# Optimization experiments

Measured on AMD Instinct MI355X. Metric: run time of the kernel, lower is better.

Reference implementation:

```python
import jax, jax.numpy as jnp
import numpy as np

B = 128      # batch
HW = 224     # image height/width
P = 16       # patch size
D = 512      # token_dim
NH = 8       # n_heads
L = 6        # t_blocks
M = 2048     # mlp_layer_size
NC = 10      # output classes
GP = HW // P            # patches per side
T = GP * GP + 1         # tokens incl. class token (197)
EPS = 1e-5


def _ln(x, g, b):
    m = jnp.mean(x, axis=-1, keepdims=True)
    v = jnp.mean(jnp.square(x - m), axis=-1, keepdims=True)
    return (x - m) / jnp.sqrt(v + EPS) * g + b


def setup_inputs() -> dict:
    key = jax.random.key(0)
    ks = iter(jax.random.split(key, 32))
    s = 0.02
    inp = {
        "images": jax.random.normal(next(ks), (B, 1, HW, HW), dtype=jnp.float32),
        "lin_map_w": jax.random.normal(next(ks), (D, P * P), dtype=jnp.float32) * s,
        "lin_map_b": jnp.zeros((D,), jnp.float32),
        "class_token": jax.random.uniform(next(ks), (1, D), dtype=jnp.float32),
        "ln1_g": jnp.ones((L, D), jnp.float32),
        "ln1_b": jnp.zeros((L, D), jnp.float32),
        "ln2_g": jnp.ones((L, D), jnp.float32),
        "ln2_b": jnp.zeros((L, D), jnp.float32),
        "qw": jax.random.normal(next(ks), (L, NH, D, D), dtype=jnp.float32) * s,
        "qb": jnp.zeros((L, NH, D), jnp.float32),
        "kw": jax.random.normal(next(ks), (L, NH, D, D), dtype=jnp.float32) * s,
        "kb": jnp.zeros((L, NH, D), jnp.float32),
        "vw": jax.random.normal(next(ks), (L, NH, D, D), dtype=jnp.float32) * s,
        "vb": jnp.zeros((L, NH, D), jnp.float32),
        "map_w": jax.random.normal(next(ks), (L, T, T * NH), dtype=jnp.float32) * s,
        "map_b": jnp.zeros((L, T), jnp.float32),
        "mlp_w1": jax.random.normal(next(ks), (L, M, D), dtype=jnp.float32) * s,
        "mlp_b1": jnp.zeros((L, M), jnp.float32),
        "mlp_w2": jax.random.normal(next(ks), (L, D, M), dtype=jnp.float32) * s,
        "mlp_b2": jnp.zeros((L, D), jnp.float32),
        "cls_w": jax.random.normal(next(ks), (NC, D), dtype=jnp.float32) * s,
        "cls_b": jnp.zeros((NC,), jnp.float32),
    }
    return inp


def reference(images, lin_map_w, lin_map_b, class_token, ln1_g, ln1_b, ln2_g, ln2_b,
              qw, qb, kw, kb, vw, vb, map_w, map_b,
              mlp_w1, mlp_b1, mlp_w2, mlp_b2, cls_w, cls_b):
    n = images.shape[0]
    img = images[:, 0]  # (B, HW, HW), channel squeezed as in patching_func
    # non-overlapping patch extraction (patchify with step=patch_size)
    patches = img.reshape(n, GP, P, GP, P).transpose(0, 1, 3, 2, 4).reshape(n, GP * GP, P * P)
    emb = patches @ lin_map_w.T + lin_map_b                 # (B, nP, D)
    cls = jnp.broadcast_to(class_token, (n, 1, D))
    x = jnp.concatenate([cls, emb], axis=1)                 # (B, T, D)
    scale = 1.0 / np.sqrt(T - 1)                            # quirky scale from source
    for l in range(L):
        h = _ln(x, ln1_g[l], ln1_b[l])
        q = jnp.einsum('btd,hed->bhte', h, qw[l]) + qb[l][None, :, None, :]
        k = jnp.einsum('btd,hed->bhte', h, kw[l]) + kb[l][None, :, None, :]
        v = jnp.einsum('btd,hed->bhte', h, vw[l]) + vb[l][None, :, None, :]
        attn = jax.nn.softmax(jnp.einsum('bhte,bhse->bhts', q, k) * scale, axis=-1)
        av = jnp.einsum('bhts,bhse->bhte', attn, v)         # (B, NH, T, D)
        res = av.reshape(n, NH * T, D)                      # head-major concat along tokens
        msa = jnp.einsum('bmd,tm->btd', res, map_w[l]) + map_b[l][None, :, None]
        x = x + msa
        y = _ln(x, ln2_g[l], ln2_b[l])
        mlp = jax.nn.gelu(y @ mlp_w1[l].T + mlp_b1[l], approximate=False) @ mlp_w2[l].T + mlp_b2[l]
        x = y + mlp                                         # note: residual uses ln2(x), per source
    logits = x[:, 0] @ cls_w.T + cls_b
    return jax.nn.softmax(logits, axis=-1)
```

## Files before the change

### kernel.cpp

```cpp
#include <hip/hip_runtime.h>
#include <hip/hip_bf16.h>
#include <math.h>

#define B_   128
#define HW_  224
#define P_   16
#define D_   512
#define NH_  8
#define L_   6
#define M_   2048
#define NC_  10
#define GP_  14
#define T_   197
#define TP_  224
#define EPS_ 1e-5f
#define ZVW2_ 2048
#define RCW_ 448

typedef __hip_bfloat16 bf16;
typedef __attribute__((ext_vector_type(8))) __bf16 bf16x8;
typedef __attribute__((ext_vector_type(4))) float  f32x4;

__device__ __forceinline__ void gload16(const void* g, void* l) {
    __builtin_amdgcn_global_load_lds(
        (const __attribute__((address_space(1))) void*)g,
        (__attribute__((address_space(3))) void*)l, 16, 0, 0);
}


__global__ void k_f32_to_bf16v(const float* __restrict__ in, bf16* __restrict__ out, long n8) {
    long stride = (long)gridDim.x * blockDim.x;
    for (long i = (long)blockIdx.x * blockDim.x + threadIdx.x; i < n8; i += stride) {
        float4 a = ((const float4*)in)[i * 2], b = ((const float4*)in)[i * 2 + 1];
        union { uint4 u; bf16 h[8]; } r;
        r.h[0] = __float2bfloat16(a.x); r.h[1] = __float2bfloat16(a.y);
        r.h[2] = __float2bfloat16(a.z); r.h[3] = __float2bfloat16(a.w);
        r.h[4] = __float2bfloat16(b.x); r.h[5] = __float2bfloat16(b.y);
        r.h[6] = __float2bfloat16(b.z); r.h[7] = __float2bfloat16(b.w);
        ((uint4*)out)[i] = r.u;
    }
}

__global__ void k_f32_to_bf16v2(const float* __restrict__ in1, bf16* __restrict__ out1,
                                const float* __restrict__ in2, bf16* __restrict__ out2, long n8) {
    long stride = (long)gridDim.x * blockDim.x;
    for (long i = (long)blockIdx.x * blockDim.x + threadIdx.x; i < n8; i += stride) {
        {
            float4 a = ((const float4*)in1)[i * 2], b = ((const float4*)in1)[i * 2 + 1];
            union { uint4 u; bf16 h[8]; } r;
            r.h[0] = __float2bfloat16(a.x); r.h[1] = __float2bfloat16(a.y);
            r.h[2] = __float2bfloat16(a.z); r.h[3] = __float2bfloat16(a.w);
            r.h[4] = __float2bfloat16(b.x); r.h[5] = __float2bfloat16(b.y);
            r.h[6] = __float2bfloat16(b.z); r.h[7] = __float2bfloat16(b.w);
            ((uint4*)out1)[i] = r.u;
        }
        {
            float4 a = ((const float4*)in2)[i * 2], b = ((const float4*)in2)[i * 2 + 1];
            union { uint4 u; bf16 h[8]; } r;
            r.h[0] = __float2bfloat16(a.x); r.h[1] = __float2bfloat16(a.y);
            r.h[2] = __float2bfloat16(a.z); r.h[3] = __float2bfloat16(a.w);
            r.h[4] = __float2bfloat16(b.x); r.h[5] = __float2bfloat16(b.y);
            r.h[6] = __float2bfloat16(b.z); r.h[7] = __float2bfloat16(b.w);
            ((uint4*)out2)[i] = r.u;
        }
    }
}

__global__ void k_prep_wv(const float* __restrict__ vw, bf16* __restrict__ wzv) {
    int idx = blockIdx.x * blockDim.x + threadIdx.x;
    if (idx >= NH_ * D_ * (D_ / 8)) return;
    int d8 = idx & 63;
    int e  = (idx >> 6) & 511;
    int h  = idx >> 15;
    long so = ((long)(h * D_ + e)) * D_ + d8 * 8;
    float4 a = *(const float4*)(vw + so), b = *(const float4*)(vw + so + 4);
    union { uint4 u; bf16 hh[8]; } rr;
    rr.hh[0] = __float2bfloat16(a.x); rr.hh[1] = __float2bfloat16(a.y);
    rr.hh[2] = __float2bfloat16(a.z); rr.hh[3] = __float2bfloat16(a.w);
    rr.hh[4] = __float2bfloat16(b.x); rr.hh[5] = __float2bfloat16(b.y);
    rr.hh[6] = __float2bfloat16(b.z); rr.hh[7] = __float2bfloat16(b.w);
    ((uint4*)wzv)[((long)(h * 1024 + 512 + e)) * 64 + d8] = rr.u;
}

__global__ __launch_bounds__(256) void k_prep_ub(const float* __restrict__ kw,
        const float* __restrict__ qb, const float* __restrict__ vb, float* __restrict__ out) {
    int gw = blockIdx.x * 4 + (threadIdx.x >> 6);
    int lane = threadIdx.x & 63;
    if (gw < NH_ * 512) {
        int h = gw >> 9, j = gw & 511;
        const float* kwh = kw + (long)h * D_ * D_ + j;
        const float* qbh = qb + h * D_;
        float s = 0.f;
#pragma unroll
        for (int i = 0; i < 8; i++) {
            int e = i * 64 + lane;
            s += kwh[(long)e * D_] * qbh[e];
        }
#pragma unroll
        for (int off = 32; off; off >>= 1) s += __shfl_xor(s, off, 64);
        if (lane == 0) out[h * 1024 + j] = s;
    } else {
        int t = (gw - NH_ * 512) * 64 + lane;
        if (t < NH_ * 512) {
            int h = t >> 9, j = t & 511;
            out[h * 1024 + 512 + j] = vb[h * D_ + j];
        }
    }
}

__global__ void k_patchify(const float* __restrict__ img, bf16* __restrict__ patches) {
    long idx = (long)blockIdx.x * blockDim.x + threadIdx.x;
    long total = (long)B_ * 196 * 256;
    if (idx >= total) return;
    int q = (int)(idx & 255);
    int p = (int)((idx >> 8) % 196);
    int b = (int)(idx / (196 * 256));
    int gy = p / GP_, gx = p % GP_;
    int py = q >> 4,  px = q & 15;
    patches[idx] = __float2bfloat16(img[((long)b * HW_ + gy * P_ + py) * HW_ + gx * P_ + px]);
}

__global__ void k_cls_token(const float* __restrict__ tok, float* __restrict__ x) {
    int i = blockIdx.x * blockDim.x + threadIdx.x;
    if (i < B_ * D_) {
        int b = i >> 9, d = i & 511;
        x[(long)b * T_ * D_ + d] = tok[d];
    }
}

__global__ void k_prep_map(const float* __restrict__ in, bf16* __restrict__ out) {
    int idx = blockIdx.x * blockDim.x + threadIdx.x;
    int total = NH_ * T_ * TP_;
    if (idx >= total) return;
    int s = idx % TP_;
    int t = (idx / TP_) % T_;
    int h = idx / (TP_ * T_);
    float v = (s < T_) ? in[t * (T_ * NH_) + h * T_ + s] : 0.f;
    out[idx] = __float2bfloat16(v);
}


template<int WRITE_Y>
__global__ __launch_bounds__(256) void k_ln(const float* x,
        const float* __restrict__ g, const float* __restrict__ bb,
        bf16* __restrict__ obf, float* of, int rows) {
    int wid = blockIdx.x * 4 + (threadIdx.x >> 6);
    if (wid >= rows) return;
    int lane = threadIdx.x & 63;
    const float* xr = x + (long)wid * D_;
    float v[8];
    float s = 0.f;
#pragma unroll
    for (int i = 0; i < 8; i++) { v[i] = xr[i * 64 + lane]; s += v[i]; }
#pragma unroll
    for (int off = 32; off; off >>= 1) s += __shfl_xor(s, off, 64);
    float mean = s * (1.f / D_);
    float sq = 0.f;
#pragma unroll
    for (int i = 0; i < 8; i++) { float d = v[i] - mean; sq += d * d; }
#pragma unroll
    for (int off = 32; off; off >>= 1) sq += __shfl_xor(sq, off, 64);
    float inv = rsqrtf(sq * (1.f / D_) + EPS_);
#pragma unroll
    for (int i = 0; i < 8; i++) {
        int d = i * 64 + lane;
        float val = (v[i] - mean) * inv * g[d] + bb[d];
        obf[(long)wid * D_ + d] = __float2bfloat16(val);
        if (WRITE_Y) of[(long)wid * D_ + d] = val;
    }
}


__global__ __launch_bounds__(256) void k_attn_ssm2(
        const bf16* __restrict__ Qbase, long ldq, long qImg, long qHead,
        const bf16* __restrict__ Kbase, long ldk, long kImg,
        bf16* __restrict__ Pm, float scale) {
    __shared__ __align__(16) bf16 Qs[128][32];
    __shared__ __align__(16) bf16 Ks[256][32];
    int z = blockIdx.z;
    int img = z & 127, h2 = z >> 7;
    int q0 = blockIdx.y * 128;
    int tid = threadIdx.x;
    int wv = tid >> 6, lane = tid & 63;

    const bf16* Qp = Qbase + (long)img * qImg + (long)h2 * qHead;
    const bf16* Kp = Kbase + (long)img * kImg;

    int sRow = 16 * wv + (lane >> 2);
    int sCol = ((lane & 3) ^ ((lane >> 3) & 3)) * 8;
    const bf16* gQ = Qp + (long)(q0 + sRow) * ldq + sCol;
    const bf16* gK = Kp + (long)sRow * ldk + sCol;
    char* lQ = (char*)Qs + (16 * wv) * 64;
    char* lK = (char*)Ks + (16 * wv) * 64;

    f32x4 acc[2][13];
#pragma unroll
    for (int j = 0; j < 2; j++)
#pragma unroll
        for (int f = 0; f < 13; f++) acc[j][f] = (f32x4){0.f, 0.f, 0.f, 0.f};

    int kgrp = lane >> 4;
#pragma unroll
    for (int kt = 0; kt < 16; kt++) {
        long k0 = (long)kt * 32;
        gload16(gQ + k0, lQ);
        gload16(gQ + 64 * ldq + k0, lQ + 4096);
#pragma unroll
        for (int p = 0; p < 4; p++)
            gload16(gK + (long)(p * 64) * ldk + k0, lK + p * 4096);
        __syncthreads();
        bf16x8 af[2];
#pragma unroll
        for (int j = 0; j < 2; j++) {
            int R = wv * 32 + j * 16 + (lane & 15);
            af[j] = *(const bf16x8*)&Qs[R][(kgrp ^ ((R >> 1) & 3)) * 8];
        }
#pragma unroll
        for (int f = 0; f < 13; f++) {
            int R = f * 16 + (lane & 15);
            bf16x8 bfr = *(const bf16x8*)&Ks[R][(kgrp ^ ((R >> 1) & 3)) * 8];
            acc[0][f] = __builtin_amdgcn_mfma_f32_16x16x32_bf16(af[0], bfr, acc[0][f], 0, 0, 0);
            acc[1][f] = __builtin_amdgcn_mfma_f32_16x16x32_bf16(af[1], bfr, acc[1][f], 0, 0, 0);
        }
        __syncthreads();
    }

    int c1 = lane & 15, grp = lane >> 4;
    const bf16 z0 = __float2bfloat16(0.f);
#pragma unroll
    for (int j = 0; j < 2; j++) {
        float mx[4] = {-1e30f, -1e30f, -1e30f, -1e30f};
        float sm[4] = {0.f, 0.f, 0.f, 0.f};
#pragma unroll
        for (int f = 0; f < 13; f++) {
            bool val = (f * 16 + c1 < T_);
#pragma unroll
            for (int r = 0; r < 4; r++) {
                float v = val ? acc[j][f][r] * scale : -1e30f;
                acc[j][f][r] = v;
                mx[r] = fmaxf(mx[r], v);
            }
        }
#pragma unroll
        for (int r = 0; r < 4; r++)
#pragma unroll
            for (int off = 1; off < 16; off <<= 1) mx[r] = fmaxf(mx[r], __shfl_xor(mx[r], off, 64));
#pragma unroll
        for (int f = 0; f < 13; f++) {
            bool val = (f * 16 + c1 < T_);
#pragma unroll
            for (int r = 0; r < 4; r++) {
                float e = val ? expf(acc[j][f][r] - mx[r]) : 0.f;
                acc[j][f][r] = e;
                sm[r] += e;
            }
        }
#pragma unroll
        for (int r = 0; r < 4; r++) {
#pragma unroll
            for (int off = 1; off < 16; off <<= 1) sm[r] += __shfl_xor(sm[r], off, 64);
            sm[r] = 1.f / sm[r];
        }
#pragma unroll
        for (int r = 0; r < 4; r++) {
            int qi = q0 + wv * 32 + j * 16 + grp * 4 + r;
            if (qi >= T_) continue;
            bf16* prow = Pm + ((long)z * T_ + qi) * TP_;
#pragma unroll
            for (int f = 0; f < 13; f++)
                prow[f * 16 + c1] = __float2bfloat16(acc[j][f][r] * sm[r]);
            prow[208 + c1] = z0;
        }
    }
}


__device__ __forceinline__ float geluf(float v) {
    return 0.5f * v * (1.f + erff(v * 0.70710678118654752f));
}

template<int MODE, bool GUARD, bool SWZ, int KT>
__global__ __launch_bounds__(256) void k_gemm_bt(
        const bf16* __restrict__ A, long lda, long bsA,
        const bf16* __restrict__ Bw, long ldb, long bsB,
        void* __restrict__ Cp, long ldc, long bsC,
        const float* __restrict__ bias,
        const float* res, long ldres,
        int Mt, int Nt) {
    __shared__ __align__(16) bf16 As[128][32];
    __shared__ __align__(16) bf16 Bs[128][32];
    int bz = blockIdx.z;
    A  += (long)bz * bsA;
    Bw += (long)bz * bsB;

    unsigned bx = blockIdx.x, by = blockIdx.y;
    if (SWZ) {
        unsigned nx = gridDim.x;
        unsigned nwg = nx * gridDim.y;
        unsigned f = by * nx + bx;
        unsigned q = nwg >> 3, r = nwg & 7;
        unsigned xcd = f & 7, idx = f >> 3;
        unsigned base = (xcd < r) ? xcd * (q + 1) : r * (q + 1) + (xcd - r) * q;
        unsigned nf = base + idx;
        bx = nf % nx;
        by = nf / nx;
    }
    int m0 = by * 128, n0 = bx * 128;

    int tid = threadIdx.x;
    int wv = tid >> 6, lane = tid & 63;
    int wm = (wv >> 1) * 64, wn = (wv & 1) * 64;
    int lrow = lane & 15, kgrp = lane >> 4;

    int rA = tid >> 2;
    int pA = (((tid & 3) ^ ((tid >> 3) & 3))) * 8;
    const bf16* gA0 = A  + (long)(m0 + rA) * lda + pA;
    const bf16* gA1 = A  + (long)(m0 + 64 + rA) * lda + pA;
    const bf16* gB0 = Bw + (long)(n0 + rA) * ldb + pA;
    const bf16* gB1 = Bw + (long)(n0 + 64 + rA) * ldb + pA;
    char* lA0 = (char*)As + (wv * 64) * 16;
    char* lA1 = (char*)As + (256 + wv * 64) * 16;
    char* lB0 = (char*)Bs + (wv * 64) * 16;
    char* lB1 = (char*)Bs + (256 + wv * 64) * 16;

    f32x4 acc[4][4];
#pragma unroll
    for (int i = 0; i < 4; i++)
#pragma unroll
        for (int j = 0; j < 4; j++) acc[i][j] = (f32x4){0.f, 0.f, 0.f, 0.f};

#pragma unroll
    for (int kt = 0; kt < (KT >> 5); kt++) {
        const long k0 = (long)kt << 5;
        gload16(gA0 + k0, lA0);
        gload16(gA1 + k0, lA1);
        gload16(gB0 + k0, lB0);
        gload16(gB1 + k0, lB1);
        __syncthreads();
        bf16x8 af[4], bfr[4];
#pragma unroll
        for (int mi = 0; mi < 4; mi++) {
            int R = wm + mi * 16 + lrow;
            af[mi] = *(const bf16x8*)&As[R][(kgrp ^ ((R >> 1) & 3)) * 8];
        }
#pragma unroll
        for (int ni = 0; ni < 4; ni++) {
            int R = wn + ni * 16 + lrow;
            bfr[ni] = *(const bf16x8*)&Bs[R][(kgrp ^ ((R >> 1) & 3)) * 8];
        }
#pragma unroll
        for (int mi = 0; mi < 4; mi++)
#pragma unroll
            for (int ni = 0; ni < 4; ni++)
                acc[mi][ni] = __builtin_amdgcn_mfma_f32_16x16x32_bf16(af[mi], bfr[ni], acc[mi][ni], 0, 0, 0);
        __syncthreads();
    }

    int r4 = (lane >> 4) * 4, c1 = lane & 15;
    float bv[4];
#pragma unroll
    for (int ni = 0; ni < 4; ni++) {
        int col = n0 + wn + ni * 16 + c1;
        bv[ni] = (bias && (!GUARD || col < Nt)) ? bias[col] : 0.f;
    }
#pragma unroll
    for (int mi = 0; mi < 4; mi++) {
#pragma unroll
        for (int r = 0; r < 4; r++) {
            int row = m0 + wm + mi * 16 + r4 + r;
            if (GUARD && row >= Mt) continue;
            long base = (long)bz * bsC + (long)row * ldc + n0 + wn + c1;
#pragma unroll
            for (int ni = 0; ni < 4; ni++) {
                if (GUARD && (n0 + wn + ni * 16 + c1) >= Nt) continue;
                float v = acc[mi][ni][r] + bv[ni];
                long cidx = base + ni * 16;
                if (MODE == 0)      ((float*)Cp)[cidx] = v;
                else if (MODE == 1) ((bf16*)Cp)[cidx]  = __float2bfloat16(v);
                else if (MODE == 2) ((bf16*)Cp)[cidx]  = __float2bfloat16(geluf(v));
                else                ((float*)Cp)[cidx] = v + res[(long)row * ldres + n0 + wn + c1 + ni * 16];
            }
        }
    }
}

__global__ __launch_bounds__(256) void k_gemm_r(
        const bf16* __restrict__ mapPair,
        const bf16* __restrict__ Pb,
        bf16* __restrict__ Rcat) {
    __shared__ __align__(16) bf16 As[128][32];
    __shared__ __align__(16) bf16 Bs[128][32];
    int z = blockIdx.z;
    int img = z & 127, h2 = z >> 7;
    const bf16* A  = mapPair + (long)h2 * T_ * TP_;
    const bf16* Bw = Pb + ((long)(h2 * 128 + img)) * (long)T_ * TP_;
    bf16* Cp = Rcat + (long)img * 224 * RCW_ + h2 * 224;
    int m0 = blockIdx.y * 128, n0 = blockIdx.x * 128;
    int tid = threadIdx.x;
    int wv = tid >> 6, lane = tid & 63;
    int wm = (wv >> 1) * 64, wn = (wv & 1) * 64;
    int lrow = lane & 15, koff = (lane >> 4) * 8;

    int rA = tid >> 2, pA = (tid & 3) * 8;
    const bf16* gA0 = A + (long)(m0 + rA) * TP_ + pA;
    const bf16* gA1 = A + (long)(m0 + 64 + rA) * TP_ + pA;
    char* lA0 = (char*)As + (wv * 64) * 16;
    char* lA1 = (char*)As + (256 + wv * 64) * 16;
    int bk = tid & 31, bg = tid >> 5;

    f32x4 acc[4][4];
#pragma unroll
    for (int i = 0; i < 4; i++)
#pragma unroll
        for (int j = 0; j < 4; j++) acc[i][j] = (f32x4){0.f, 0.f, 0.f, 0.f};

#pragma unroll
    for (int kt = 0; kt < 7; kt++) {
        long k0 = (long)kt << 5;
        gload16(gA0 + k0, lA0);
        gload16(gA1 + k0, lA1);
#pragma unroll
        for (int i = 0; i < 2; i++) {
            int g = bg + 8 * i;
            uint4 v = *(const uint4*)(Bw + (k0 + bk) * TP_ + n0 + g * 8);
            const bf16* pv = (const bf16*)&v;
#pragma unroll
            for (int j = 0; j < 8; j++) Bs[g * 8 + j][bk] = pv[j];
        }
        __syncthreads();
        bf16x8 af[4], bfr[4];
#pragma unroll
        for (int mi = 0; mi < 4; mi++) af[mi]  = *(const bf16x8*)&As[wm + mi * 16 + lrow][koff];
#pragma unroll
        for (int ni = 0; ni < 4; ni++) bfr[ni] = *(const bf16x8*)&Bs[wn + ni * 16 + lrow][koff];
#pragma unroll
        for (int mi = 0; mi < 4; mi++)
#pragma unroll
            for (int ni = 0; ni < 4; ni++)
                acc[mi][ni] = __builtin_amdgcn_mfma_f32_16x16x32_bf16(af[mi], bfr[ni], acc[mi][ni], 0, 0, 0);
        __syncthreads();
    }

    int r4 = (lane >> 4) * 4, c1 = lane & 15;
#pragma unroll
    for (int mi = 0; mi < 4; mi++) {
#pragma unroll
        for (int r = 0; r < 4; r++) {
            int row = m0 + wm + mi * 16 + r4 + r;
            if (row >= T_) continue;
#pragma unroll
            for (int ni = 0; ni < 4; ni++) {
                int col = n0 + wn + ni * 16 + c1;
                if (col >= 224) continue;
                Cp[(long)row * RCW_ + col] = __float2bfloat16(acc[mi][ni][r]);
            }
        }
    }
}

__global__ __launch_bounds__(256) void k_gemm_rv(
        const bf16* __restrict__ Rcat,
        const bf16* __restrict__ ZV,
        float* __restrict__ xf,
        const float* __restrict__ rowbias) {
    __shared__ __align__(16) bf16 As[128][32];
    __shared__ __align__(16) bf16 Bs[128][32];
    int img = blockIdx.z;
    const bf16* A = Rcat + (long)img * 224 * RCW_;
    const bf16* Vimg = ZV + (long)img * T_ * ZVW2_;
    float* Cp = xf + (long)img * T_ * D_;
    int m0 = blockIdx.y * 128, n0 = blockIdx.x * 128;
    int tid = threadIdx.x;
    int wv = tid >> 6, lane = tid & 63;
    int wm = (wv >> 1) * 64, wn = (wv & 1) * 64;
    int lrow = lane & 15, koff = (lane >> 4) * 8;

    int rA = tid >> 2, pA = (tid & 3) * 8;
    const bf16* gA0 = A + (long)(m0 + rA) * RCW_ + pA;
    const bf16* gA1 = A + (long)(m0 + 64 + rA) * RCW_ + pA;
    char* lA0 = (char*)As + (wv * 64) * 16;
    char* lA1 = (char*)As + (256 + wv * 64) * 16;
    int bk = tid & 31, bg = tid >> 5;

    f32x4 acc[4][4];
#pragma unroll
    for (int i = 0; i < 4; i++)
#pragma unroll
        for (int j = 0; j < 4; j++) acc[i][j] = (f32x4){0.f, 0.f, 0.f, 0.f};

#pragma unroll
    for (int kt = 0; kt < 14; kt++) {
        long k0 = (long)kt << 5;
        gload16(gA0 + k0, lA0);
        gload16(gA1 + k0, lA1);
        const bf16* Vb = (kt < 7) ? (Vimg + 512 + k0 * ZVW2_)
                                  : (Vimg + 1536 + (k0 - 224) * ZVW2_);
#pragma unroll
        for (int i = 0; i < 2; i++) {
            int g = bg + 8 * i;
            uint4 v = *(const uint4*)(Vb + (long)bk * ZVW2_ + n0 + g * 8);
            const bf16* pv = (const bf16*)&v;
#pragma unroll
            for (int j = 0; j < 8; j++) Bs[g * 8 + j][bk] = pv[j];
        }
        __syncthreads();
        bf16x8 af[4], bfr[4];
#pragma unroll
        for (int mi = 0; mi < 4; mi++) af[mi]  = *(const bf16x8*)&As[wm + mi * 16 + lrow][koff];
#pragma unroll
        for (int ni = 0; ni < 4; ni++) bfr[ni] = *(const bf16x8*)&Bs[wn + ni * 16 + lrow][koff];
#pragma unroll
        for (int mi = 0; mi < 4; mi++)
#pragma unroll
            for (int ni = 0; ni < 4; ni++)
                acc[mi][ni] = __builtin_amdgcn_mfma_f32_16x16x32_bf16(af[mi], bfr[ni], acc[mi][ni], 0, 0, 0);
        __syncthreads();
    }

    int r4 = (lane >> 4) * 4, c1 = lane & 15;
#pragma unroll
    for (int mi = 0; mi < 4; mi++) {
#pragma unroll
        for (int r = 0; r < 4; r++) {
            int row = m0 + wm + mi * 16 + r4 + r;
            if (row >= T_) continue;
            float rb = rowbias ? rowbias[row] : 0.f;
#pragma unroll
            for (int ni = 0; ni < 4; ni++) {
                int col = n0 + wn + ni * 16 + c1;
                Cp[(long)row * D_ + col] += acc[mi][ni][r] + rb * 0.25f;
            }
        }
    }
}

__global__ __launch_bounds__(256) void k_gemm_tn(
        const bf16* __restrict__ A, long lda, long bsA,
        const bf16* __restrict__ Bw, long ldb, long bsB,
        bf16* __restrict__ Cp, long ldc, long bsC,
        int Mt, int Nt, int Kt) {
    __shared__ __align__(16) bf16 As[128][32];
    __shared__ __align__(16) bf16 Bs[128][32];
    int bz = blockIdx.z;
    A  += (long)bz * bsA;
    Bw += (long)bz * bsB;
    int m0 = blockIdx.y * 128, n0 = blockIdx.x * 128;
    int tid = threadIdx.x;
    int wv = tid >> 6, lane = tid & 63;
    int wm = (wv >> 1) * 64, wn = (wv & 1) * 64;
    int lrow = lane & 15, koff = (lane >> 4) * 8;
    int bk = tid & 31, bg = tid >> 5;

    f32x4 acc[4][4];
#pragma unroll
    for (int i = 0; i < 4; i++)
#pragma unroll
        for (int j = 0; j < 4; j++) acc[i][j] = (f32x4){0.f, 0.f, 0.f, 0.f};

    int kTiles = Kt >> 5;
    for (int kt = 0; kt < kTiles; kt++) {
        long k0 = (long)kt << 5;
#pragma unroll
        for (int i = 0; i < 2; i++) {
            int g = bg + 8 * i;
            uint4 va = *(const uint4*)(A + (k0 + bk) * lda + m0 + g * 8);
            const bf16* pa = (const bf16*)&va;
#pragma unroll
            for (int j = 0; j < 8; j++) As[g * 8 + j][bk] = pa[j];
            uint4 vb = *(const uint4*)(Bw + (k0 + bk) * ldb + n0 + g * 8);
            const bf16* pb = (const bf16*)&vb;
#pragma unroll
            for (int j = 0; j < 8; j++) Bs[g * 8 + j][bk] = pb[j];
        }
        __syncthreads();
        bf16x8 af[4], bfr[4];
#pragma unroll
        for (int mi = 0; mi < 4; mi++) af[mi]  = *(const bf16x8*)&As[wm + mi * 16 + lrow][koff];
#pragma unroll
        for (int ni = 0; ni < 4; ni++) bfr[ni] = *(const bf16x8*)&Bs[wn + ni * 16 + lrow][koff];
#pragma unroll
        for (int mi = 0; mi < 4; mi++)
#pragma unroll
            for (int ni = 0; ni < 4; ni++)
                acc[mi][ni] = __builtin_amdgcn_mfma_f32_16x16x32_bf16(af[mi], bfr[ni], acc[mi][ni], 0, 0, 0);
        __syncthreads();
    }

    int r4 = (lane >> 4) * 4, c1 = lane & 15;
#pragma unroll
    for (int mi = 0; mi < 4; mi++) {
#pragma unroll
        for (int r = 0; r < 4; r++) {
            int row = m0 + wm + mi * 16 + r4 + r;
            if (row >= Mt) continue;
#pragma unroll
            for (int ni = 0; ni < 4; ni++) {
                int col = n0 + wn + ni * 16 + c1;
                if (col >= Nt) continue;
                Cp[(long)bz * bsC + (long)row * ldc + col] = __float2bfloat16(acc[mi][ni][r]);
            }
        }
    }
}


__global__ __launch_bounds__(64) void k_classifier(const float* __restrict__ x,
        const float* __restrict__ w, const float* __restrict__ bias, float* __restrict__ out) {
    int b = blockIdx.x, lane = threadIdx.x;
    const float* xr = x + (long)b * T_ * D_;
    float logits[NC_];
#pragma unroll
    for (int c = 0; c < NC_; c++) {
        float s = 0.f;
        for (int d = lane; d < D_; d += 64) s += xr[d] * w[c * D_ + d];
#pragma unroll
        for (int off = 32; off; off >>= 1) s += __shfl_xor(s, off, 64);
        logits[c] = s + bias[c];
    }
    float mx = -1e30f;
#pragma unroll
    for (int c = 0; c < NC_; c++) mx = fmaxf(mx, logits[c]);
    float sum = 0.f;
#pragma unroll
    for (int c = 0; c < NC_; c++) { float e = expf(logits[c] - mx); logits[c] = e; sum += e; }
    if (lane == 0) {
        float inv = 1.f / sum;
#pragma unroll
        for (int c = 0; c < NC_; c++) out[(long)b * NC_ + c] = logits[c] * inv;
    }
}


extern "C" void kernel_launch(void* const* d_in, const int* in_sizes, int n_in,
                              void* d_out, int out_size, void* d_ws, size_t ws_size,
                              hipStream_t stream) {
    const float* images  = (const float*)d_in[0];
    const float* lin_w   = (const float*)d_in[1];
    const float* lin_b   = (const float*)d_in[2];
    const float* cls_tok = (const float*)d_in[3];
    const float* ln1_g   = (const float*)d_in[4];
    const float* ln1_b   = (const float*)d_in[5];
    const float* ln2_g   = (const float*)d_in[6];
    const float* ln2_b   = (const float*)d_in[7];
    const float* qw      = (const float*)d_in[8];
    const float* qb      = (const float*)d_in[9];
    const float* kw      = (const float*)d_in[10];
    const float* kb      = (const float*)d_in[11];
    const float* vw      = (const float*)d_in[12];
    const float* vb      = (const float*)d_in[13];
    const float* map_w   = (const float*)d_in[14];
    const float* map_b   = (const float*)d_in[15];
    const float* w1      = (const float*)d_in[16];
    const float* b1      = (const float*)d_in[17];
    const float* w2      = (const float*)d_in[18];
    const float* b2      = (const float*)d_in[19];
    const float* cls_w   = (const float*)d_in[20];
    const float* cls_b   = (const float*)d_in[21];

    char* wp = (char*)d_ws;
    auto alloc = [&](size_t bytes) { char* p = wp; wp += (bytes + 255) & ~(size_t)255; return p; };
    const long BT = (long)B_ * T_;

    float* xf   = (float*)alloc(BT * D_ * 4);
    bf16*  hb   = (bf16*) alloc((BT + 192) * D_ * 2);
    bf16*  ZVh2 = (bf16*) alloc((size_t)(BT + 160) * ZVW2_ * 2);
    bf16*  m1c  = ZVh2;
    bf16*  Pb2  = (bf16*) alloc(((size_t)256 * T_ + 64) * TP_ * 2);
    char*  rcReg= alloc(((size_t)128 * 224 + 64) * RCW_ * 2);
    bf16*  Rcat = (bf16*)rcReg;
    bf16*  patches = (bf16*)rcReg;
    bf16*  wqb  = (bf16*)rcReg;
    bf16*  wkb  = (bf16*)(rcReg + (long)NH_ * D_ * D_ * 2);
    bf16*  wzv  = (bf16*) alloc(((long)NH_ * 1024 + 64) * D_ * 2);
    float* zvb  = (float*)alloc((long)NH_ * 1024 * 4);
    bf16*  wmapP= (bf16*) alloc(((long)NH_ * T_ + 64) * TP_ * 2);
    bf16*  w1l  = (bf16*) alloc((long)(M_ + 64) * D_ * 2);
    bf16*  w2l  = (bf16*) alloc((long)(D_ + 64) * M_ * 2);
    bf16*  wlin = (bf16*) alloc((long)(D_ + 64) * 256 * 2);

    k_f32_to_bf16v<<<1024, 256, 0, stream>>>(lin_w, wlin, (long)D_ * 256 / 8);
    {
        long tot = (long)B_ * 196 * 256;
        k_patchify<<<(int)((tot + 255) / 256), 256, 0, stream>>>(images, patches);
        k_cls_token<<<(B_ * D_ + 255) / 256, 256, 0, stream>>>(cls_tok, xf);
        k_gemm_bt<0, true, false, 256><<<dim3(4, 2, B_), 256, 0, stream>>>(
            patches, 256, (long)196 * 256,
            wlin, 256, 0,
            xf + D_, D_, (long)T_ * D_,
            lin_b, nullptr, 0,
            196, D_);
    }

    const float scale = 1.0f / 14.0f;
    const int lnGrid = (int)((BT + 3) / 4);

    for (int l = 0; l < L_; l++) {
        k_f32_to_bf16v2<<<1024, 256, 0, stream>>>(
            qw + (long)l * NH_ * D_ * D_, wqb,
            kw + (long)l * NH_ * D_ * D_, wkb, (long)NH_ * D_ * D_ / 8);
        k_gemm_tn<<<dim3(4, 4, NH_), 256, 0, stream>>>(
            wkb, D_, (long)D_ * D_,
            wqb, D_, (long)D_ * D_,
            wzv, D_, (long)1024 * D_,
            D_, D_, D_);
        k_prep_wv<<<(NH_ * D_ * (D_ / 8) + 255) / 256, 256, 0, stream>>>(
            vw + (long)l * NH_ * D_ * D_, wzv);
        k_prep_ub<<<(NH_ * 512 + NH_ * 8 + 3) / 4, 256, 0, stream>>>(
            kw + (long)l * NH_ * D_ * D_, qb + (long)l * NH_ * D_,
            vb + (long)l * NH_ * D_, zvb);
        k_f32_to_bf16v2<<<1024, 256, 0, stream>>>(
            w1 + (long)l * M_ * D_, w1l,
            w2 + (long)l * D_ * M_, w2l, (long)M_ * D_ / 8);
        k_prep_map<<<(NH_ * T_ * TP_ + 255) / 256, 256, 0, stream>>>(
            map_w + (long)l * T_ * T_ * NH_, wmapP);

        k_ln<0><<<lnGrid, 256, 0, stream>>>(xf, ln1_g + l * D_, ln1_b + l * D_, hb, nullptr, (int)BT);

        for (int hp = 0; hp < 4; hp++) {
            k_gemm_bt<1, false, true, 512><<<dim3(16, 197, 1), 256, 0, stream>>>(
                hb, D_, 0, wzv + (long)hp * 2048 * D_, D_, 0,
                ZVh2, ZVW2_, 0, zvb + (long)hp * 2048, nullptr, 0,
                (int)BT, ZVW2_);

            k_attn_ssm2<<<dim3(1, 2, 256), 256, 0, stream>>>(
                ZVh2, ZVW2_, (long)T_ * ZVW2_, 1024,
                hb, D_, (long)T_ * D_,
                Pb2, scale);

            k_gemm_r<<<dim3(2, 2, 256), 256, 0, stream>>>(
                wmapP + (long)(hp * 2) * T_ * TP_, Pb2, Rcat);

            k_gemm_rv<<<dim3(4, 2, B_), 256, 0, stream>>>(
                Rcat, ZVh2, xf, map_b + (long)l * T_);
        }

        k_ln<1><<<lnGrid, 256, 0, stream>>>(xf, ln2_g + l * D_, ln2_b + l * D_, hb, xf, (int)BT);

        k_gemm_bt<2, false, true, 512><<<dim3(16, 197, 1), 256, 0, stream>>>(
            hb, D_, 0, w1l, D_, 0,
            m1c, M_, 0, b1 + (long)l * M_, nullptr, 0, (int)BT, M_);
        k_gemm_bt<3, false, true, 2048><<<dim3(4, 197, 1), 256, 0, stream>>>(
            m1c, M_, 0, w2l, M_, 0,
            xf, D_, 0, b2 + (long)l * D_, xf, D_, (int)BT, D_);
    }

    k_classifier<<<B_, 64, 0, stream>>>(xf, cls_w, cls_b, (float*)d_out);
}
```

Before: 7.199 ms.

## Triple-buffer LDS tiles in bf16 GEMM with async global-to-LDS prefetch

```diff
diff --git a/kernel.cpp b/kernel.cpp
--- a/kernel.cpp
+++ b/kernel.cpp
@@ -27,6 +27,8 @@
         (__attribute__((address_space(3))) void*)l, 16, 0, 0);
 }
 
+#define SCHED0_ __builtin_amdgcn_sched_barrier(0)
+
 
 __global__ void k_f32_to_bf16v(const float* __restrict__ in, bf16* __restrict__ out, long n8) {
     long stride = (long)gridDim.x * blockDim.x;
@@ -287,8 +289,8 @@
         const float* __restrict__ bias,
         const float* res, long ldres,
         int Mt, int Nt) {
-    __shared__ __align__(16) bf16 As[128][32];
-    __shared__ __align__(16) bf16 Bs[128][32];
+    __shared__ __align__(16) bf16 As[3][128][32];
+    __shared__ __align__(16) bf16 Bs[3][128][32];
     int bz = blockIdx.z;
     A  += (long)bz * bsA;
     Bw += (long)bz * bsB;
@@ -323,38 +325,51 @@
     char* lB0 = (char*)Bs + (wv * 64) * 16;
     char* lB1 = (char*)Bs + (256 + wv * 64) * 16;
 
+    auto stage = [&](int buf, int kt) {
+        const long k0 = (long)kt << 5;
+        const int bo = buf * 8192;
+        gload16(gA0 + k0, lA0 + bo);
+        gload16(gA1 + k0, lA1 + bo);
+        gload16(gB0 + k0, lB0 + bo);
+        gload16(gB1 + k0, lB1 + bo);
+    };
+
     f32x4 acc[4][4];
 #pragma unroll
     for (int i = 0; i < 4; i++)
 #pragma unroll
         for (int j = 0; j < 4; j++) acc[i][j] = (f32x4){0.f, 0.f, 0.f, 0.f};
 
+    stage(0, 0);
+    stage(1, 1);
+    asm volatile("s_waitcnt vmcnt(4)" ::: "memory");
+    SCHED0_; __builtin_amdgcn_s_barrier(); SCHED0_;
+
 #pragma unroll
     for (int kt = 0; kt < (KT >> 5); kt++) {
-        const long k0 = (long)kt << 5;
-        gload16(gA0 + k0, lA0);
-        gload16(gA1 + k0, lA1);
-        gload16(gB0 + k0, lB0);
-        gload16(gB1 + k0, lB1);
-        __syncthreads();
+        stage((kt + 2) % 3, kt + 2);
+        const int c = kt % 3;
         bf16x8 af[4], bfr[4];
 #pragma unroll
         for (int mi = 0; mi < 4; mi++) {
             int R = wm + mi * 16 + lrow;
-            af[mi] = *(const bf16x8*)&As[R][(kgrp ^ ((R >> 1) & 3)) * 8];
+            af[mi] = *(const bf16x8*)&As[c][R][(kgrp ^ ((R >> 1) & 3)) * 8];
         }
 #pragma unroll
         for (int ni = 0; ni < 4; ni++) {
             int R = wn + ni * 16 + lrow;
-            bfr[ni] = *(const bf16x8*)&Bs[R][(kgrp ^ ((R >> 1) & 3)) * 8];
+            bfr[ni] = *(const bf16x8*)&Bs[c][R][(kgrp ^ ((R >> 1) & 3)) * 8];
         }
 #pragma unroll
         for (int mi = 0; mi < 4; mi++)
 #pragma unroll
             for (int ni = 0; ni < 4; ni++)
                 acc[mi][ni] = __builtin_amdgcn_mfma_f32_16x16x32_bf16(af[mi], bfr[ni], acc[mi][ni], 0, 0, 0);
-        __syncthreads();
-    }
+        SCHED0_;
+        asm volatile("s_waitcnt vmcnt(4)" ::: "memory");
+        SCHED0_; __builtin_amdgcn_s_barrier(); SCHED0_;
+    }
+    asm volatile("s_waitcnt vmcnt(0)" ::: "memory");
 
     int r4 = (lane >> 4) * 4, c1 = lane & 15;
     float bv[4];
```

After: 7.218 ms. Within noise of the previous version (+0.3%).
